# Kernel optimization log

Hardware: AMD Instinct MI355X
Metric: run time of the kernel (lower is better)

## Reference

```python
import jax, jax.numpy as jnp
import numpy as np

B, LQ, LK = 4, 128, 1024
Q_SIZE, K_SIZE, V_SIZE, UNITS = 512, 512, 512, 256
MASK_VAL = -1e6  # matches torch masked_softmax value=-1000000.0


def setup_inputs() -> dict:
    key = jax.random.key(0)
    ks = jax.random.split(key, 7)
    return {
        "query": jax.random.normal(ks[0], (B, LQ, Q_SIZE), dtype=jnp.float32),
        "key": jax.random.normal(ks[1], (B, LK, K_SIZE), dtype=jnp.float32),
        "value": jax.random.normal(ks[2], (B, LK, V_SIZE), dtype=jnp.float32),
        "valid_len": jax.random.randint(ks[3], (B,), 1, LK + 1).astype(jnp.int64),
        # torch nn.Linear(in, out, bias=False) weight is (out, in)
        "W_q": jax.random.normal(ks[4], (UNITS, Q_SIZE), dtype=jnp.float32) / np.sqrt(Q_SIZE),
        "W_k": jax.random.normal(ks[5], (UNITS, K_SIZE), dtype=jnp.float32) / np.sqrt(K_SIZE),
        "v": jax.random.normal(ks[6], (UNITS,), dtype=jnp.float32) / np.sqrt(UNITS),
    }


def reference(query, key, value, valid_len, W_q, W_k, v):
    # projections: (B,Lq,units), (B,Lk,units)
    q = jnp.einsum("bqd,ud->bqu", query, W_q)
    k = jnp.einsum("bkd,ud->bku", key, W_k)
    # additive features: (B,Lq,Lk,units)
    feats = jnp.tanh(q[:, :, None, :] + k[:, None, :, :])
    # v-projection -> scores (B,Lq,Lk)
    scores = jnp.einsum("bqku,u->bqk", feats, v)
    # mask positions >= valid_len with -1e6 (same as torch sequence_mask)
    mask = jnp.arange(scores.shape[-1]) < valid_len[:, None, None]
    scores = jnp.where(mask, scores, MASK_VAL)
    attn = jax.nn.softmax(scores, axis=-1)  # dropout rate is 0.0
    return jnp.einsum("bqk,bkv->bqv", attn, value)
```

## Files before the change

### kernel.cpp

```cpp
#include <hip/hip_runtime.h>


typedef _Float16 half8 __attribute__((ext_vector_type(8)));
typedef float floatx4 __attribute__((ext_vector_type(4)));

#define EQ_OFF   0
#define EKT_OFF  (512 * 256)
#define ATTN_OFF (EKT_OFF + 4 * 256 * 1024)

__global__ __launch_bounds__(256) void proj_mfma(
    const float* __restrict__ query, const float* __restrict__ key,
    const float* __restrict__ W_q, const float* __restrict__ W_k,
    const int* __restrict__ vlen, float* __restrict__ Eq,
    float* __restrict__ EkT) {
  __shared__ __align__(16) _Float16 As[64 * 32];
  __shared__ __align__(16) _Float16 Bs[64 * 32];
  const int tid = threadIdx.x;
  const int mb = blockIdx.x;
  const int u0 = blockIdx.y * 64;
  const bool qpart = mb < 8;
  const float *Ag, *Bg;
  int kbatch = 0, j0 = 0, m0 = 0;
  if (qpart) {
    m0 = mb * 64;
    Ag = query + (size_t)m0 * 512;
    Bg = W_q + (size_t)u0 * 512;
  } else {
    const int g0 = (mb - 8) * 64;
    kbatch = g0 >> 10;
    j0 = g0 & 1023;
    if (j0 >= vlen[kbatch]) return;
    Ag = W_k + (size_t)u0 * 512;
    Bg = key + (size_t)g0 * 512;
  }

  const int lrow = tid >> 2, lkq = (tid & 3) * 8;
  const float* Ags = Ag + lrow * 512 + lkq;
  const float* Bgs = Bg + lrow * 512 + lkq;
  _Float16* Ads = As + lrow * 32 + lkq;
  _Float16* Bds = Bs + lrow * 32 + lkq;

  const int lane = tid & 63;
  const int wid = tid >> 6;
  const int wm = (wid & 1) * 32, wn = (wid >> 1) * 32;
  const int frow = lane & 15;
  const int fk = (lane >> 4) * 8;

  floatx4 acc[2][2] = {{{0.f, 0.f, 0.f, 0.f}, {0.f, 0.f, 0.f, 0.f}},
                       {{0.f, 0.f, 0.f, 0.f}, {0.f, 0.f, 0.f, 0.f}}};

  float4 ra0 = *(const float4*)Ags;
  float4 ra1 = *(const float4*)(Ags + 4);
  float4 rb0 = *(const float4*)Bgs;
  float4 rb1 = *(const float4*)(Bgs + 4);

  for (int kb = 0; kb < 16; ++kb) {
    half8 ha, hb;
    ha[0] = (_Float16)ra0.x; ha[1] = (_Float16)ra0.y;
    ha[2] = (_Float16)ra0.z; ha[3] = (_Float16)ra0.w;
    ha[4] = (_Float16)ra1.x; ha[5] = (_Float16)ra1.y;
    ha[6] = (_Float16)ra1.z; ha[7] = (_Float16)ra1.w;
    hb[0] = (_Float16)rb0.x; hb[1] = (_Float16)rb0.y;
    hb[2] = (_Float16)rb0.z; hb[3] = (_Float16)rb0.w;
    hb[4] = (_Float16)rb1.x; hb[5] = (_Float16)rb1.y;
    hb[6] = (_Float16)rb1.z; hb[7] = (_Float16)rb1.w;
    __syncthreads();
    *(half8*)Ads = ha;
    *(half8*)Bds = hb;
    __syncthreads();
    if (kb + 1 < 16) {
      ra0 = *(const float4*)(Ags + (kb + 1) * 32);
      ra1 = *(const float4*)(Ags + (kb + 1) * 32 + 4);
      rb0 = *(const float4*)(Bgs + (kb + 1) * 32);
      rb1 = *(const float4*)(Bgs + (kb + 1) * 32 + 4);
    }
    half8 a0 = *(const half8*)(As + (wm + frow) * 32 + fk);
    half8 a1 = *(const half8*)(As + (wm + 16 + frow) * 32 + fk);
    half8 b0 = *(const half8*)(Bs + (wn + frow) * 32 + fk);
    half8 b1 = *(const half8*)(Bs + (wn + 16 + frow) * 32 + fk);
    acc[0][0] = __builtin_amdgcn_mfma_f32_16x16x32_f16(a0, b0, acc[0][0], 0, 0, 0);
    acc[0][1] = __builtin_amdgcn_mfma_f32_16x16x32_f16(a0, b1, acc[0][1], 0, 0, 0);
    acc[1][0] = __builtin_amdgcn_mfma_f32_16x16x32_f16(a1, b0, acc[1][0], 0, 0, 0);
    acc[1][1] = __builtin_amdgcn_mfma_f32_16x16x32_f16(a1, b1, acc[1][1], 0, 0, 0);
  }

  const int rbase = (lane >> 4) * 4;
  const int col = lane & 15;
#pragma unroll
  for (int mi = 0; mi < 2; ++mi)
#pragma unroll
    for (int ni = 0; ni < 2; ++ni)
#pragma unroll
      for (int r = 0; r < 4; ++r) {
        const int R = wm + mi * 16 + rbase + r;
        const int C = wn + ni * 16 + col;
        const float e = __expf(2.f * acc[mi][ni][r]);
        if (qpart)
          Eq[(m0 + R) * 256 + u0 + C] = e;
        else
          EkT[kbatch * 262144 + (u0 + R) * 1024 + j0 + C] = e;
      }
}

__device__ __forceinline__ float block_reduce16(float v, int op, float* red) {
#pragma unroll
  for (int off = 32; off > 0; off >>= 1) {
    float o = __shfl_xor(v, off, 64);
    v = op ? fmaxf(v, o) : (v + o);
  }
  __syncthreads();
  if ((threadIdx.x & 63) == 0) red[threadIdx.x >> 6] = v;
  __syncthreads();
  float r = red[0];
#pragma unroll
  for (int i = 1; i < 16; ++i) r = op ? fmaxf(r, red[i]) : (r + red[i]);
  return r;
}

__global__ __launch_bounds__(1024) void scores_softmax(
    const float* __restrict__ Eq, const float* __restrict__ EkT,
    const float* __restrict__ vvec, const int* __restrict__ valid_len,
    float* __restrict__ attn) {
  __shared__ float4 QV[256];
  __shared__ float red[16];
  const int tid = threadIdx.x;
  const int b = blockIdx.x >> 6;
  const int i0 = (blockIdx.x & 63) * 2;
  const int vl = valid_len[b];

  float vv = 0.f;
  if (tid < 256) {
    vv = vvec[tid];
    QV[tid] = make_float4(Eq[(b * 128 + i0) * 256 + tid],
                          Eq[(b * 128 + i0 + 1) * 256 + tid], -2.f * vv, 0.f);
  }
  const float SV = block_reduce16(vv, 0, red);

  const int j = tid;
  float s0 = -1e6f, s1 = -1e6f;
  if (j < vl) {
    float a0 = 0.f, a1 = 0.f;
    const float* kp = EkT + b * 262144 + j;
#pragma unroll 8
    for (int u = 0; u < 256; ++u) {
      float ek = kp[u << 10];
      float4 q = QV[u];
      float r0 = __builtin_amdgcn_rcpf(fmaf(q.x, ek, 1.f));
      float r1 = __builtin_amdgcn_rcpf(fmaf(q.y, ek, 1.f));
      a0 = fmaf(q.z, r0, a0);
      a1 = fmaf(q.z, r1, a1);
    }
    s0 = SV + a0;
    s1 = SV + a1;
  }

  float M0 = block_reduce16(s0, 1, red);
  float p0 = (j < vl) ? __expf(s0 - M0) : 0.f;
  float S0 = block_reduce16(p0, 0, red);
  attn[(b * 128 + i0) * 1024 + j] = p0 * __builtin_amdgcn_rcpf(S0);

  float M1 = block_reduce16(s1, 1, red);
  float p1 = (j < vl) ? __expf(s1 - M1) : 0.f;
  float S1 = block_reduce16(p1, 0, red);
  attn[(b * 128 + i0 + 1) * 1024 + j] = p1 * __builtin_amdgcn_rcpf(S1);
}

__global__ __launch_bounds__(512) void attn_value(
    const float* __restrict__ attn, const float* __restrict__ value,
    const int* __restrict__ valid_len, float* __restrict__ out) {
  __shared__ float red[8][8][64];
  const int bid = blockIdx.x;
  const int b = bid >> 7;
  const int rg = (bid >> 3) & 15;
  const int cg = bid & 7;
  const int i0 = rg * 8;
  const int w = threadIdx.x >> 6;
  const int lane = threadIdx.x & 63;
  const int vl = valid_len[b];
  const float* A = attn + (b * 128 + i0) * 1024;
  const float* V = value + b * 524288 + cg * 64 + lane;

  float acc[8] = {};
  const int kstart = w * 128;
  const int kend = min(kstart + 128, vl);
  int k = kstart;
  for (; k + 8 <= kend; k += 8) {
#pragma unroll
    for (int t = 0; t < 8; ++t) {
      float vx = V[(k + t) * 512];
#pragma unroll
      for (int r = 0; r < 8; ++r) acc[r] = fmaf(A[r * 1024 + k + t], vx, acc[r]);
    }
  }
  for (; k < kend; ++k) {
    float vx = V[k * 512];
#pragma unroll
    for (int r = 0; r < 8; ++r) acc[r] = fmaf(A[r * 1024 + k], vx, acc[r]);
  }

#pragma unroll
  for (int r = 0; r < 8; ++r) red[w][r][lane] = acc[r];
  __syncthreads();
  const int r = threadIdx.x >> 6;
  float s = 0.f;
#pragma unroll
  for (int ww = 0; ww < 8; ++ww) s += red[ww][r][lane];
  out[(b * 128 + i0 + r) * 512 + cg * 64 + lane] = s;
}

extern "C" void kernel_launch(void* const* d_in, const int* in_sizes, int n_in,
                              void* d_out, int out_size, void* d_ws, size_t ws_size,
                              hipStream_t stream) {
  const float* query = (const float*)d_in[0];
  const float* key   = (const float*)d_in[1];
  const float* value = (const float*)d_in[2];
  const int*   vlen  = (const int*)d_in[3];
  const float* W_q   = (const float*)d_in[4];
  const float* W_k   = (const float*)d_in[5];
  const float* v     = (const float*)d_in[6];
  float* out = (float*)d_out;

  float* ws   = (float*)d_ws;
  float* Eq   = ws + EQ_OFF;
  float* EkT  = ws + EKT_OFF;
  float* attn = ws + ATTN_OFF;

  proj_mfma<<<dim3(72, 4), 256, 0, stream>>>(query, key, W_q, W_k, vlen, Eq, EkT);
  scores_softmax<<<256, 1024, 0, stream>>>(Eq, EkT, v, vlen, attn);
  attn_value<<<512, 512, 0, stream>>>(attn, value, vlen, out);
}
```

Measured before the change: 125.4 us.

## Register-block score kernel over two keys, drop max pass, vectorize attn loads

The scores kernel now runs 512 threads, each computing two adjacent key columns for both query rows. It loads EkT as float2 and reuses each shared-memory QV entry across four outputs. The softmax max reduction is removed and the constant v-sum is accumulated inside the loop, cutting the kernel down to a single block-wide sum reduction. attn_value loads attention rows as float4 and value rows four at a time. Skipping the max subtraction assumes scores stay small enough for exp not to overflow, and the smaller blocks halve the number of threads in flight.

After: 128.9 us. +2.8%, slower.

```diff
diff --git a/kernel.cpp b/kernel.cpp
--- a/kernel.cpp
+++ b/kernel.cpp
@@ -102,67 +102,65 @@
       }
 }
 
-__device__ __forceinline__ float block_reduce16(float v, int op, float* red) {
-#pragma unroll
-  for (int off = 32; off > 0; off >>= 1) {
-    float o = __shfl_xor(v, off, 64);
-    v = op ? fmaxf(v, o) : (v + o);
-  }
-  __syncthreads();
-  if ((threadIdx.x & 63) == 0) red[threadIdx.x >> 6] = v;
-  __syncthreads();
-  float r = red[0];
-#pragma unroll
-  for (int i = 1; i < 16; ++i) r = op ? fmaxf(r, red[i]) : (r + red[i]);
-  return r;
-}
-
-__global__ __launch_bounds__(1024) void scores_softmax(
+__global__ __launch_bounds__(512) void scores_softmax(
     const float* __restrict__ Eq, const float* __restrict__ EkT,
     const float* __restrict__ vvec, const int* __restrict__ valid_len,
     float* __restrict__ attn) {
   __shared__ float4 QV[256];
-  __shared__ float red[16];
+  __shared__ float2 red[8];
   const int tid = threadIdx.x;
   const int b = blockIdx.x >> 6;
   const int i0 = (blockIdx.x & 63) * 2;
   const int vl = valid_len[b];
 
-  float vv = 0.f;
   if (tid < 256) {
-    vv = vvec[tid];
+    float vv = vvec[tid];
     QV[tid] = make_float4(Eq[(b * 128 + i0) * 256 + tid],
-                          Eq[(b * 128 + i0 + 1) * 256 + tid], -2.f * vv, 0.f);
-  }
-  const float SV = block_reduce16(vv, 0, red);
-
-  const int j = tid;
-  float s0 = -1e6f, s1 = -1e6f;
-  if (j < vl) {
-    float a0 = 0.f, a1 = 0.f;
-    const float* kp = EkT + b * 262144 + j;
-#pragma unroll 8
+                          Eq[(b * 128 + i0 + 1) * 256 + tid], -2.f * vv, vv);
+  }
+  __syncthreads();
+
+  const int j0 = tid * 2;
+  float s00 = 0.f, s01 = 0.f, s10 = 0.f, s11 = 0.f;
+  if (j0 < vl) {
+    float a00 = 0.f, a01 = 0.f, a10 = 0.f, a11 = 0.f, sv = 0.f;
+    const float2* kp = (const float2*)(EkT + b * 262144) + tid;
+#pragma unroll 4
     for (int u = 0; u < 256; ++u) {
-      float ek = kp[u << 10];
+      float2 ek = kp[u << 9];
       float4 q = QV[u];
-      float r0 = __builtin_amdgcn_rcpf(fmaf(q.x, ek, 1.f));
-      float r1 = __builtin_amdgcn_rcpf(fmaf(q.y, ek, 1.f));
-      a0 = fmaf(q.z, r0, a0);
-      a1 = fmaf(q.z, r1, a1);
+      sv += q.w;
+      float r00 = __builtin_amdgcn_rcpf(fmaf(q.x, ek.x, 1.f));
+      float r01 = __builtin_amdgcn_rcpf(fmaf(q.x, ek.y, 1.f));
+      float r10 = __builtin_amdgcn_rcpf(fmaf(q.y, ek.x, 1.f));
+      float r11 = __builtin_amdgcn_rcpf(fmaf(q.y, ek.y, 1.f));
+      a00 = fmaf(q.z, r00, a00);
+      a01 = fmaf(q.z, r01, a01);
+      a10 = fmaf(q.z, r10, a10);
+      a11 = fmaf(q.z, r11, a11);
     }
-    s0 = SV + a0;
-    s1 = SV + a1;
-  }
-
-  float M0 = block_reduce16(s0, 1, red);
-  float p0 = (j < vl) ? __expf(s0 - M0) : 0.f;
-  float S0 = block_reduce16(p0, 0, red);
-  attn[(b * 128 + i0) * 1024 + j] = p0 * __builtin_amdgcn_rcpf(S0);
-
-  float M1 = block_reduce16(s1, 1, red);
-  float p1 = (j < vl) ? __expf(s1 - M1) : 0.f;
-  float S1 = block_reduce16(p1, 0, red);
-  attn[(b * 128 + i0 + 1) * 1024 + j] = p1 * __builtin_amdgcn_rcpf(S1);
+    s00 = sv + a00; s01 = sv + a01; s10 = sv + a10; s11 = sv + a11;
+  }
+  float p00 = (j0 < vl) ? __expf(s00) : 0.f;
+  float p01 = (j0 + 1 < vl) ? __expf(s01) : 0.f;
+  float p10 = (j0 < vl) ? __expf(s10) : 0.f;
+  float p11 = (j0 + 1 < vl) ? __expf(s11) : 0.f;
+
+  float2 ss = make_float2(p00 + p01, p10 + p11);
+#pragma unroll
+  for (int off = 32; off > 0; off >>= 1) {
+    ss.x += __shfl_xor(ss.x, off, 64);
+    ss.y += __shfl_xor(ss.y, off, 64);
+  }
+  if ((tid & 63) == 0) red[tid >> 6] = ss;
+  __syncthreads();
+  float Sx = 0.f, Sy = 0.f;
+#pragma unroll
+  for (int w = 0; w < 8; ++w) { Sx += red[w].x; Sy += red[w].y; }
+  const float rs0 = __builtin_amdgcn_rcpf(Sx);
+  const float rs1 = __builtin_amdgcn_rcpf(Sy);
+  *(float2*)(attn + (b * 128 + i0) * 1024 + j0) = make_float2(p00 * rs0, p01 * rs0);
+  *(float2*)(attn + (b * 128 + i0 + 1) * 1024 + j0) = make_float2(p10 * rs1, p11 * rs1);
 }
 
 __global__ __launch_bounds__(512) void attn_value(
@@ -181,18 +179,26 @@
   const float* V = value + b * 524288 + cg * 64 + lane;
 
   float acc[8] = {};
-  const int kstart = w * 128;
-  const int kend = min(kstart + 128, vl);
-  int k = kstart;
-  for (; k + 8 <= kend; k += 8) {
-#pragma unroll
-    for (int t = 0; t < 8; ++t) {
-      float vx = V[(k + t) * 512];
-#pragma unroll
-      for (int r = 0; r < 8; ++r) acc[r] = fmaf(A[r * 1024 + k + t], vx, acc[r]);
+  const int ks = w * 128;
+  const int ke = min(ks + 128, vl);
+  int k = ks;
+  for (; k + 4 <= ke; k += 4) {
+    float4 a[8];
+#pragma unroll
+    for (int r = 0; r < 8; ++r) a[r] = *(const float4*)(A + r * 1024 + k);
+    float v0 = V[k * 512];
+    float v1 = V[(k + 1) * 512];
+    float v2 = V[(k + 2) * 512];
+    float v3 = V[(k + 3) * 512];
+#pragma unroll
+    for (int r = 0; r < 8; ++r) {
+      acc[r] = fmaf(a[r].x, v0, acc[r]);
+      acc[r] = fmaf(a[r].y, v1, acc[r]);
+      acc[r] = fmaf(a[r].z, v2, acc[r]);
+      acc[r] = fmaf(a[r].w, v3, acc[r]);
     }
   }
-  for (; k < kend; ++k) {
+  for (; k < ke; ++k) {
     float vx = V[k * 512];
 #pragma unroll
     for (int r = 0; r < 8; ++r) acc[r] = fmaf(A[r * 1024 + k], vx, acc[r]);
@@ -226,6 +232,6 @@
   float* attn = ws + ATTN_OFF;
 
   proj_mfma<<<dim3(72, 4), 256, 0, stream>>>(query, key, W_q, W_k, vlen, Eq, EkT);
-  scores_softmax<<<256, 1024, 0, stream>>>(Eq, EkT, v, vlen, attn);
+  scores_softmax<<<256, 512, 0, stream>>>(Eq, EkT, v, vlen, attn);
   attn_value<<<512, 512, 0, stream>>>(attn, value, vlen, out);
 }
```

## Fuse softmax and attention-value product into the scores kernel

Applied to the files above, without the earlier changes.

Merges the scores/softmax kernel and the attention-times-value kernel into one. Unnormalized probabilities stay in shared memory, and each block then multiplies its two rows against the value matrix, normalizing at the end. This removes the attention matrix round trip through global memory and one kernel launch. It also drops the max-subtraction reduction, relying on the scores being bounded by the sum of |v|. The catch is that every block now rereads the full value slice for its batch, with a long, serial, latency-bound accumulation loop.

Measured after the change: 129.3 us. 3.1% more time.

```diff
diff --git a/kernel.cpp b/kernel.cpp
--- a/kernel.cpp
+++ b/kernel.cpp
@@ -6,7 +6,6 @@
 
 #define EQ_OFF   0
 #define EKT_OFF  (512 * 256)
-#define ATTN_OFF (EKT_OFF + 4 * 256 * 1024)
 
 __global__ __launch_bounds__(256) void proj_mfma(
     const float* __restrict__ query, const float* __restrict__ key,
@@ -102,110 +101,75 @@
       }
 }
 
-__device__ __forceinline__ float block_reduce16(float v, int op, float* red) {
-#pragma unroll
-  for (int off = 32; off > 0; off >>= 1) {
-    float o = __shfl_xor(v, off, 64);
-    v = op ? fmaxf(v, o) : (v + o);
-  }
-  __syncthreads();
-  if ((threadIdx.x & 63) == 0) red[threadIdx.x >> 6] = v;
-  __syncthreads();
-  float r = red[0];
-#pragma unroll
-  for (int i = 1; i < 16; ++i) r = op ? fmaxf(r, red[i]) : (r + red[i]);
-  return r;
-}
-
-__global__ __launch_bounds__(1024) void scores_softmax(
+__global__ __launch_bounds__(1024) void scores_attn(
     const float* __restrict__ Eq, const float* __restrict__ EkT,
     const float* __restrict__ vvec, const int* __restrict__ valid_len,
-    float* __restrict__ attn) {
+    const float* __restrict__ value, float* __restrict__ out) {
   __shared__ float4 QV[256];
-  __shared__ float red[16];
+  __shared__ float P0[1024];
+  __shared__ float P1[1024];
+  __shared__ float2 red[16];
   const int tid = threadIdx.x;
   const int b = blockIdx.x >> 6;
   const int i0 = (blockIdx.x & 63) * 2;
   const int vl = valid_len[b];
 
-  float vv = 0.f;
   if (tid < 256) {
-    vv = vvec[tid];
+    float vv = vvec[tid];
     QV[tid] = make_float4(Eq[(b * 128 + i0) * 256 + tid],
-                          Eq[(b * 128 + i0 + 1) * 256 + tid], -2.f * vv, 0.f);
+                          Eq[(b * 128 + i0 + 1) * 256 + tid], -2.f * vv, vv);
   }
-  const float SV = block_reduce16(vv, 0, red);
+  __syncthreads();
 
   const int j = tid;
-  float s0 = -1e6f, s1 = -1e6f;
+  float p0 = 0.f, p1 = 0.f;
   if (j < vl) {
-    float a0 = 0.f, a1 = 0.f;
+    float a0 = 0.f, a1 = 0.f, sv = 0.f;
     const float* kp = EkT + b * 262144 + j;
 #pragma unroll 8
     for (int u = 0; u < 256; ++u) {
       float ek = kp[u << 10];
       float4 q = QV[u];
+      sv += q.w;
       float r0 = __builtin_amdgcn_rcpf(fmaf(q.x, ek, 1.f));
       float r1 = __builtin_amdgcn_rcpf(fmaf(q.y, ek, 1.f));
       a0 = fmaf(q.z, r0, a0);
       a1 = fmaf(q.z, r1, a1);
     }
-    s0 = SV + a0;
-    s1 = SV + a1;
+    p0 = __expf(sv + a0);
+    p1 = __expf(sv + a1);
   }
+  P0[j] = p0;
+  P1[j] = p1;
 
-  float M0 = block_reduce16(s0, 1, red);
-  float p0 = (j < vl) ? __expf(s0 - M0) : 0.f;
-  float S0 = block_reduce16(p0, 0, red);
-  attn[(b * 128 + i0) * 1024 + j] = p0 * __builtin_amdgcn_rcpf(S0);
+  float2 pp = make_float2(p0, p1);
+#pragma unroll
+  for (int off = 32; off > 0; off >>= 1) {
+    pp.x += __shfl_xor(pp.x, off, 64);
+    pp.y += __shfl_xor(pp.y, off, 64);
+  }
+  if ((tid & 63) == 0) red[tid >> 6] = pp;
+  __syncthreads();
+  float den0 = 0.f, den1 = 0.f;
+#pragma unroll
+  for (int w = 0; w < 16; ++w) { den0 += red[w].x; den1 += red[w].y; }
 
-  float M1 = block_reduce16(s1, 1, red);
-  float p1 = (j < vl) ? __expf(s1 - M1) : 0.f;
-  float S1 = block_reduce16(p1, 0, red);
-  attn[(b * 128 + i0 + 1) * 1024 + j] = p1 * __builtin_amdgcn_rcpf(S1);
-}
-
-__global__ __launch_bounds__(512) void attn_value(
-    const float* __restrict__ attn, const float* __restrict__ value,
-    const int* __restrict__ valid_len, float* __restrict__ out) {
-  __shared__ float red[8][8][64];
-  const int bid = blockIdx.x;
-  const int b = bid >> 7;
-  const int rg = (bid >> 3) & 15;
-  const int cg = bid & 7;
-  const int i0 = rg * 8;
-  const int w = threadIdx.x >> 6;
-  const int lane = threadIdx.x & 63;
-  const int vl = valid_len[b];
-  const float* A = attn + (b * 128 + i0) * 1024;
-  const float* V = value + b * 524288 + cg * 64 + lane;
-
-  float acc[8] = {};
-  const int kstart = w * 128;
-  const int kend = min(kstart + 128, vl);
-  int k = kstart;
-  for (; k + 8 <= kend; k += 8) {
+  const int r = tid >> 9;
+  const int c = tid & 511;
+  const float* P = r ? P1 : P0;
+  const float* Vb = value + b * 524288 + c;
+  float acc0 = 0.f, acc1 = 0.f;
+  int jj = 0;
+  for (; jj + 8 <= vl; jj += 8) {
 #pragma unroll
-    for (int t = 0; t < 8; ++t) {
-      float vx = V[(k + t) * 512];
-#pragma unroll
-      for (int r = 0; r < 8; ++r) acc[r] = fmaf(A[r * 1024 + k + t], vx, acc[r]);
+    for (int t = 0; t < 8; t += 2) {
+      acc0 = fmaf(P[jj + t], Vb[(jj + t) * 512], acc0);
+      acc1 = fmaf(P[jj + t + 1], Vb[(jj + t + 1) * 512], acc1);
     }
   }
-  for (; k < kend; ++k) {
-    float vx = V[k * 512];
-#pragma unroll
-    for (int r = 0; r < 8; ++r) acc[r] = fmaf(A[r * 1024 + k], vx, acc[r]);
-  }
-
-#pragma unroll
-  for (int r = 0; r < 8; ++r) red[w][r][lane] = acc[r];
-  __syncthreads();
-  const int r = threadIdx.x >> 6;
-  float s = 0.f;
-#pragma unroll
-  for (int ww = 0; ww < 8; ++ww) s += red[ww][r][lane];
-  out[(b * 128 + i0 + r) * 512 + cg * 64 + lane] = s;
+  for (; jj < vl; ++jj) acc0 = fmaf(P[jj], Vb[jj * 512], acc0);
+  const float rden = __builtin_amdgcn_rcpf(r ? den1 : den0);
+  out[(b * 128 + i0 + r) * 512 + c] = (acc0 + acc1) * rden;
 }
 
 extern "C" void kernel_launch(void* const* d_in, const int* in_sizes, int n_in,
@@ -220,12 +184,10 @@
   const float* v     = (const float*)d_in[6];
   float* out = (float*)d_out;
 
-  float* ws   = (float*)d_ws;
-  float* Eq   = ws + EQ_OFF;
-  float* EkT  = ws + EKT_OFF;
-  float* attn = ws + ATTN_OFF;
+  float* ws  = (float*)d_ws;
+  float* Eq  = ws + EQ_OFF;
+  float* EkT = ws + EKT_OFF;
 
   proj_mfma<<<dim3(72, 4), 256, 0, stream>>>(query, key, W_q, W_k, vlen, Eq, EkT);
-  scores_softmax<<<256, 1024, 0, stream>>>(Eq, EkT, v, vlen, attn);
-  attn_value<<<512, 512, 0, stream>>>(attn, value, vlen, out);
+  scores_attn<<<256, 1024, 0, stream>>>(Eq, EkT, v, vlen, value, out);
 }
```

## Drop softmax max pass, fuse reductions, double-buffer proj LDS, vectorize attn loads

Applied to the files above, without the earlier changes.

Softmax now skips the max-subtraction because scores are bounded by the norm of v, and it reduces both rows' denominators in one float2 block reduction. This cuts the number of block-wide barriers. The projection GEMM double-buffers its shared tiles to remove one barrier per k-step. The attention-value kernel loads attention weights as float4. The block index mapping is also permuted to interleave batches. Dropping the max relies on scores staying small enough for exp not to overflow.

Result: faster. 116.9 us (-6.8%).

```diff
diff --git a/kernel.cpp b/kernel.cpp
--- a/kernel.cpp
+++ b/kernel.cpp
@@ -13,8 +13,8 @@
     const float* __restrict__ W_q, const float* __restrict__ W_k,
     const int* __restrict__ vlen, float* __restrict__ Eq,
     float* __restrict__ EkT) {
-  __shared__ __align__(16) _Float16 As[64 * 32];
-  __shared__ __align__(16) _Float16 Bs[64 * 32];
+  __shared__ __align__(16) _Float16 As[2][64 * 32];
+  __shared__ __align__(16) _Float16 Bs[2][64 * 32];
   const int tid = threadIdx.x;
   const int mb = blockIdx.x;
   const int u0 = blockIdx.y * 64;
@@ -37,8 +37,7 @@
   const int lrow = tid >> 2, lkq = (tid & 3) * 8;
   const float* Ags = Ag + lrow * 512 + lkq;
   const float* Bgs = Bg + lrow * 512 + lkq;
-  _Float16* Ads = As + lrow * 32 + lkq;
-  _Float16* Bds = Bs + lrow * 32 + lkq;
+  const int lofs = lrow * 32 + lkq;
 
   const int lane = tid & 63;
   const int wid = tid >> 6;
@@ -55,6 +54,7 @@
   float4 rb1 = *(const float4*)(Bgs + 4);
 
   for (int kb = 0; kb < 16; ++kb) {
+    const int buf = kb & 1;
     half8 ha, hb;
     ha[0] = (_Float16)ra0.x; ha[1] = (_Float16)ra0.y;
     ha[2] = (_Float16)ra0.z; ha[3] = (_Float16)ra0.w;
@@ -64,9 +64,8 @@
     hb[2] = (_Float16)rb0.z; hb[3] = (_Float16)rb0.w;
     hb[4] = (_Float16)rb1.x; hb[5] = (_Float16)rb1.y;
     hb[6] = (_Float16)rb1.z; hb[7] = (_Float16)rb1.w;
-    __syncthreads();
-    *(half8*)Ads = ha;
-    *(half8*)Bds = hb;
+    *(half8*)(As[buf] + lofs) = ha;
+    *(half8*)(Bs[buf] + lofs) = hb;
     __syncthreads();
     if (kb + 1 < 16) {
       ra0 = *(const float4*)(Ags + (kb + 1) * 32);
@@ -74,10 +73,10 @@
       rb0 = *(const float4*)(Bgs + (kb + 1) * 32);
       rb1 = *(const float4*)(Bgs + (kb + 1) * 32 + 4);
     }
-    half8 a0 = *(const half8*)(As + (wm + frow) * 32 + fk);
-    half8 a1 = *(const half8*)(As + (wm + 16 + frow) * 32 + fk);
-    half8 b0 = *(const half8*)(Bs + (wn + frow) * 32 + fk);
-    half8 b1 = *(const half8*)(Bs + (wn + 16 + frow) * 32 + fk);
+    half8 a0 = *(const half8*)(As[buf] + (wm + frow) * 32 + fk);
+    half8 a1 = *(const half8*)(As[buf] + (wm + 16 + frow) * 32 + fk);
+    half8 b0 = *(const half8*)(Bs[buf] + (wn + frow) * 32 + fk);
+    half8 b1 = *(const half8*)(Bs[buf] + (wn + 16 + frow) * 32 + fk);
     acc[0][0] = __builtin_amdgcn_mfma_f32_16x16x32_f16(a0, b0, acc[0][0], 0, 0, 0);
     acc[0][1] = __builtin_amdgcn_mfma_f32_16x16x32_f16(a0, b1, acc[0][1], 0, 0, 0);
     acc[1][0] = __builtin_amdgcn_mfma_f32_16x16x32_f16(a1, b0, acc[1][0], 0, 0, 0);
@@ -102,30 +101,16 @@
       }
 }
 
-__device__ __forceinline__ float block_reduce16(float v, int op, float* red) {
-#pragma unroll
-  for (int off = 32; off > 0; off >>= 1) {
-    float o = __shfl_xor(v, off, 64);
-    v = op ? fmaxf(v, o) : (v + o);
-  }
-  __syncthreads();
-  if ((threadIdx.x & 63) == 0) red[threadIdx.x >> 6] = v;
-  __syncthreads();
-  float r = red[0];
-#pragma unroll
-  for (int i = 1; i < 16; ++i) r = op ? fmaxf(r, red[i]) : (r + red[i]);
-  return r;
-}
-
 __global__ __launch_bounds__(1024) void scores_softmax(
     const float* __restrict__ Eq, const float* __restrict__ EkT,
     const float* __restrict__ vvec, const int* __restrict__ valid_len,
     float* __restrict__ attn) {
   __shared__ float4 QV[256];
-  __shared__ float red[16];
+  __shared__ float2 red[16];
   const int tid = threadIdx.x;
-  const int b = blockIdx.x >> 6;
-  const int i0 = (blockIdx.x & 63) * 2;
+  const int bx = blockIdx.x;
+  const int b = (bx >> 1) & 3;
+  const int i0 = ((((bx >> 3) << 1) | (bx & 1))) * 2;
   const int vl = valid_len[b];
 
   float vv = 0.f;
@@ -134,10 +119,17 @@
     QV[tid] = make_float4(Eq[(b * 128 + i0) * 256 + tid],
                           Eq[(b * 128 + i0 + 1) * 256 + tid], -2.f * vv, 0.f);
   }
-  const float SV = block_reduce16(vv, 0, red);
+  float sv = vv;
+#pragma unroll
+  for (int off = 32; off > 0; off >>= 1) sv += __shfl_xor(sv, off, 64);
+  if ((tid & 63) == 0) red[tid >> 6] = make_float2(sv, 0.f);
+  __syncthreads();
+  float SV = 0.f;
+#pragma unroll
+  for (int w = 0; w < 16; ++w) SV += red[w].x;
 
   const int j = tid;
-  float s0 = -1e6f, s1 = -1e6f;
+  float p0 = 0.f, p1 = 0.f;
   if (j < vl) {
     float a0 = 0.f, a1 = 0.f;
     const float* kp = EkT + b * 262144 + j;
@@ -150,19 +142,25 @@
       a0 = fmaf(q.z, r0, a0);
       a1 = fmaf(q.z, r1, a1);
     }
-    s0 = SV + a0;
-    s1 = SV + a1;
-  }
-
-  float M0 = block_reduce16(s0, 1, red);
-  float p0 = (j < vl) ? __expf(s0 - M0) : 0.f;
-  float S0 = block_reduce16(p0, 0, red);
-  attn[(b * 128 + i0) * 1024 + j] = p0 * __builtin_amdgcn_rcpf(S0);
-
-  float M1 = block_reduce16(s1, 1, red);
-  float p1 = (j < vl) ? __expf(s1 - M1) : 0.f;
-  float S1 = block_reduce16(p1, 0, red);
-  attn[(b * 128 + i0 + 1) * 1024 + j] = p1 * __builtin_amdgcn_rcpf(S1);
+    p0 = __expf(SV + a0);
+    p1 = __expf(SV + a1);
+  }
+
+  float2 pp = make_float2(p0, p1);
+#pragma unroll
+  for (int off = 32; off > 0; off >>= 1) {
+    pp.x += __shfl_xor(pp.x, off, 64);
+    pp.y += __shfl_xor(pp.y, off, 64);
+  }
+  __syncthreads();
+  if ((tid & 63) == 0) red[tid >> 6] = pp;
+  __syncthreads();
+  float den0 = 0.f, den1 = 0.f;
+#pragma unroll
+  for (int w = 0; w < 16; ++w) { den0 += red[w].x; den1 += red[w].y; }
+
+  attn[(b * 128 + i0) * 1024 + j] = p0 * __builtin_amdgcn_rcpf(den0);
+  attn[(b * 128 + i0 + 1) * 1024 + j] = p1 * __builtin_amdgcn_rcpf(den1);
 }
 
 __global__ __launch_bounds__(512) void attn_value(
@@ -181,18 +179,26 @@
   const float* V = value + b * 524288 + cg * 64 + lane;
 
   float acc[8] = {};
-  const int kstart = w * 128;
-  const int kend = min(kstart + 128, vl);
-  int k = kstart;
-  for (; k + 8 <= kend; k += 8) {
-#pragma unroll
-    for (int t = 0; t < 8; ++t) {
-      float vx = V[(k + t) * 512];
-#pragma unroll
-      for (int r = 0; r < 8; ++r) acc[r] = fmaf(A[r * 1024 + k + t], vx, acc[r]);
+  const int ks = w * 128;
+  const int ke = min(ks + 128, vl);
+  int k = ks;
+  for (; k + 4 <= ke; k += 4) {
+    float4 a[8];
+#pragma unroll
+    for (int r = 0; r < 8; ++r) a[r] = *(const float4*)(A + r * 1024 + k);
+    float v0 = V[k * 512];
+    float v1 = V[(k + 1) * 512];
+    float v2 = V[(k + 2) * 512];
+    float v3 = V[(k + 3) * 512];
+#pragma unroll
+    for (int r = 0; r < 8; ++r) {
+      acc[r] = fmaf(a[r].x, v0, acc[r]);
+      acc[r] = fmaf(a[r].y, v1, acc[r]);
+      acc[r] = fmaf(a[r].z, v2, acc[r]);
+      acc[r] = fmaf(a[r].w, v3, acc[r]);
     }
   }
-  for (; k < kend; ++k) {
+  for (; k < ke; ++k) {
     float vx = V[k * 512];
 #pragma unroll
     for (int r = 0; r < 8; ++r) acc[r] = fmaf(A[r * 1024 + k], vx, acc[r]);
```
